# Optimization experiments

Hardware: AMD Instinct MI355X
Metric: run time of the kernel (lower is better)

The kernel has to match this reference:

```python
import jax, jax.numpy as jnp
import numpy as np

B, S, D, H = 2, 2048, 768, 12
HD = D // H  # head dim = 64

def setup_inputs() -> dict:
    key = jax.random.key(0)
    ks = jax.random.split(key, 9)
    s = 1.0 / np.sqrt(D)
    return {
        "x": jax.random.normal(ks[0], (B, S, D), dtype=jnp.float32),
        "Wq": jax.random.uniform(ks[1], (D, D), jnp.float32, -s, s),
        "bq": jax.random.uniform(ks[2], (D,), jnp.float32, -s, s),
        "Wk": jax.random.uniform(ks[3], (D, D), jnp.float32, -s, s),
        "bk": jax.random.uniform(ks[4], (D,), jnp.float32, -s, s),
        "Wv": jax.random.uniform(ks[5], (D, D), jnp.float32, -s, s),
        "bv": jax.random.uniform(ks[6], (D,), jnp.float32, -s, s),
        "Wo": jax.random.uniform(ks[7], (D, D), jnp.float32, -s, s),
        "bo": jax.random.uniform(ks[8], (D,), jnp.float32, -s, s),
    }

def reference(x, Wq, bq, Wk, bk, Wv, bv, Wo, bo):
    b, s, _ = x.shape
    # linear projections, split into heads: [b, h, s, hd]
    def proj(W, bias):
        y = x @ W + bias
        return y.reshape(b, s, H, HD).transpose(0, 2, 1, 3)
    q = proj(Wq, bq)
    k = proj(Wk, bk)
    v = proj(Wv, bv)
    scale = 1.0 / np.sqrt(HD).astype(np.float32)
    scores = jnp.einsum('bhqd,bhkd->bhqk', q, k) * scale
    attn = jax.nn.softmax(scores, axis=-1)
    out = jnp.einsum('bhqk,bhkd->bhqd', attn, v)
    out = out.transpose(0, 2, 1, 3).reshape(b, s, D)
    return out @ Wo + bo
```

## Files before the change

kernel.cpp:

```cpp
#include <hip/hip_runtime.h>
#include <math.h>

#define NH 12
#define SEQ 2048
#define DM 768
#define HD 64
#define NB 2
#define MT (NB * SEQ)
#define QSCL 0.18033688011112042591999058512524f

typedef short bf16x8 __attribute__((ext_vector_type(8)));
typedef float f32x16 __attribute__((ext_vector_type(16)));
typedef unsigned u32x2 __attribute__((ext_vector_type(2)));

__device__ __forceinline__ unsigned short bf16_rne(float x) {
    unsigned u = __float_as_uint(x);
    u += 0x7fffu + ((u >> 16) & 1u);
    return (unsigned short)(u >> 16);
}
__device__ __forceinline__ float bf16_tof(short h) {
    return __uint_as_float(((unsigned)(unsigned short)h) << 16);
}
__device__ __forceinline__ unsigned cvtpk(float lo, float hi) {
    unsigned r;
    asm("v_cvt_pk_bf16_f32 %0, %1, %2" : "=v"(r) : "v"(lo), "v"(hi));
    return r;
}

__device__ __forceinline__ void gl_lds16(const void* g, void* s) {
    __builtin_amdgcn_global_load_lds(
        (const __attribute__((address_space(1))) unsigned int*)g,
        (__attribute__((address_space(3))) unsigned int*)s, 16, 0, 0);
}

__device__ __forceinline__ f32x16 mfma32(bf16x8 a, bf16x8 b, f32x16 c) {
    return __builtin_amdgcn_mfma_f32_32x32x16_bf16(a, b, c, 0, 0, 0);
}

__device__ __forceinline__ bf16x8 gfrag(const char* base, int row, int physblk) {
    return *(const bf16x8*)(base + row * 64 + physblk * 16);
}
__device__ __forceinline__ bf16x8 afrag(const short* base, int row, int blk) {
    return *(const bf16x8*)(base + row * 64 + ((blk ^ (row & 7)) << 3));
}

__global__ __launch_bounds__(256)
void conv_all(const float* __restrict__ x,
              const float* __restrict__ Wq, const float* __restrict__ Wk,
              const float* __restrict__ Wv, const float* __restrict__ Wo,
              short* __restrict__ xg, short* __restrict__ wdst)
{
    int b = blockIdx.x;
    if (b < 1536) {
        const int idx = b * 256 + threadIdx.x;
        const int m = idx / 96, bk = idx % 96;
        const float* src = x + (size_t)m * DM + bk * 8;
        float4 v0 = *(const float4*)src;
        float4 v1 = *(const float4*)(src + 4);
        const float vv[8] = {v0.x, v0.y, v0.z, v0.w, v1.x, v1.y, v1.z, v1.w};
        union { short s[8]; int4 q; } hh;
#pragma unroll
        for (int j = 0; j < 8; j++) hh.s[j] = (short)bf16_rne(vv[j]);
        const int pb = (bk & ~3) | ((bk & 3) ^ ((m >> 1) & 3));
        *(int4*)(xg + (size_t)m * DM + pb * 8) = hh.q;
    } else {
        b -= 1536;
        const int z = b / 288;
        const float* __restrict__ W = (z == 0) ? Wq : (z == 1) ? Wk : (z == 2) ? Wv : Wo;
        const int idx = (b % 288) * 256 + threadIdx.x;
        const int n = idx % 768, bk = idx / 768;
        union { short s[8]; int4 q; } hh;
#pragma unroll
        for (int j = 0; j < 8; j++) hh.s[j] = (short)bf16_rne(W[(size_t)(bk * 8 + j) * DM + n]);
        const int pb = (bk & ~3) | ((bk & 3) ^ ((n >> 1) & 3));
        *(int4*)(wdst + (size_t)z * 589824 + (size_t)n * DM + pb * 8) = hh.q;
    }
}

template<bool SWAP>
__device__ __forceinline__ void qkv_loop(const char* pA, const char* pB,
                                         char* As, char* Bs,
                                         int t, f32x16* acc)
{
    const int w = t >> 6, l = t & 63;
    const int q32 = l & 31, half = l >> 5;
    const int sel = (q32 >> 1) & 3;
    const int arow  = 32 * (w & 1) + q32;
    const int brow0 = 64 * (w >> 1) + q32;
    char* dA = As + t * 16;
    char* dB = Bs + t * 16;

    uint4 a0, b00, b10;
    uint4 a1, b01, b11;

    a0  = *(const uint4*)(pA);
    b00 = *(const uint4*)(pB);
    b10 = *(const uint4*)(pB + 64 * 1536);
    a1  = *(const uint4*)(pA + 64);
    b01 = *(const uint4*)(pB + 64);
    b11 = *(const uint4*)(pB + 64 * 1536 + 64);
    *(uint4*)dA = a0;
    *(uint4*)dB = b00;
    *(uint4*)(dB + 4096) = b10;
    __syncthreads();

    auto compute = [&](const char* sA, const char* sB) {
#pragma unroll
        for (int s = 0; s < 2; s++) {
            const int blk = (s * 2 + half) ^ sel;
            bf16x8 a  = gfrag(sA, arow, blk);
            bf16x8 b0 = gfrag(sB, brow0, blk);
            bf16x8 b1 = gfrag(sB, brow0 + 32, blk);
            if (SWAP) {
                acc[0] = mfma32(b0, a, acc[0]);
                acc[1] = mfma32(b1, a, acc[1]);
            } else {
                acc[0] = mfma32(a, b0, acc[0]);
                acc[1] = mfma32(a, b1, acc[1]);
            }
        }
    };

    for (int kb = 0; kb < 12; kb++) {
        if (kb < 11) {
            const size_t cb = (size_t)(2 * kb + 2) * 64;
            a0  = *(const uint4*)(pA + cb);
            b00 = *(const uint4*)(pB + cb);
            b10 = *(const uint4*)(pB + 64 * 1536 + cb);
        }
        *(uint4*)(dA + 4096) = a1;
        *(uint4*)(dB + 8192) = b01;
        *(uint4*)(dB + 8192 + 4096) = b11;
        compute(As, Bs);
        __syncthreads();

        if (kb < 11) {
            const size_t cb = (size_t)(2 * kb + 3) * 64;
            a1  = *(const uint4*)(pA + cb);
            b01 = *(const uint4*)(pB + cb);
            b11 = *(const uint4*)(pB + 64 * 1536 + cb);
        }
        if (kb < 11) {
            *(uint4*)dA = a0;
            *(uint4*)dB = b00;
            *(uint4*)(dB + 4096) = b10;
        }
        compute(As + 4096, Bs + 8192);
        __syncthreads();
    }
}

__global__ __launch_bounds__(256)
void gemm_qkv(const short* __restrict__ xg, const short* __restrict__ wt,
              const float* __restrict__ bq, const float* __restrict__ bkv,
              const float* __restrict__ bv,
              short* __restrict__ qg, short* __restrict__ kg, short* __restrict__ vg)
{
    const int z = blockIdx.z;
    const short* __restrict__ Bw = wt + (size_t)z * 589824;
    const float* __restrict__ bias = (z == 0) ? bq : (z == 1) ? bkv : bv;

    __shared__ char As[8192], Bs[16384];
    const int t = threadIdx.x, w = t >> 6, l = t & 63;
    const int m0 = blockIdx.y * 64, n0 = blockIdx.x * 128;
    const int q32 = l & 31, half = l >> 5;

    const char* pA = (const char*)xg + (size_t)(m0 + (t >> 2)) * 1536 + (t & 3) * 16;
    const char* pB = (const char*)Bw + (size_t)(n0 + (t >> 2)) * 1536 + (t & 3) * 16;

    f32x16 acc[2];
#pragma unroll
    for (int i = 0; i < 2; i++)
#pragma unroll
        for (int r = 0; r < 16; r++) acc[i][r] = 0.f;

    if (z == 2) {
        qkv_loop<false>(pA, pB, As, Bs, t, acc);
        const int nbase = n0 + 64 * (w >> 1);
        const int h = nbase >> 6;
        const int mbase = m0 + 32 * (w & 1) + 4 * half;
        const int bb = mbase >> 11;
#pragma unroll
        for (int nt = 0; nt < 2; nt++) {
            const int hd = 32 * nt + q32;
            const float bia = bias[nbase + hd];
            short* vrow = vg + ((size_t)(bb * NH + h) * HD + hd) * SEQ;
#pragma unroll
            for (int g = 0; g < 4; g++) {
                const int ss0 = (mbase & 2047) + 8 * g;
                union { unsigned short u[4]; uint2 q; } pk;
#pragma unroll
                for (int j = 0; j < 4; j++)
                    pk.u[j] = bf16_rne(acc[nt][4 * g + j] + bia);
                const int blk = ss0 >> 3;
                const int phys = (blk & ~7) | ((blk & 7) ^ (hd & 7));
                *(uint2*)(vrow + phys * 8 + (ss0 & 7)) = pk.q;
            }
        }
    } else {
        qkv_loop<true>(pA, pB, As, Bs, t, acc);
        short* dst = (z == 0) ? qg : kg;
        const float scl = (z == 0) ? QSCL : 1.0f;
        const int mcol = m0 + 32 * (w & 1) + q32;
        const int bb = mcol >> 11, ss = mcol & 2047;
        const int h = (n0 + 64 * (w >> 1)) >> 6;
        short* drow = dst + ((size_t)(bb * NH + h) * SEQ + ss) * HD;
#pragma unroll
        for (int nt = 0; nt < 2; nt++)
#pragma unroll
            for (int g = 0; g < 4; g++) {
                const int hd0 = 32 * nt + 8 * g + 4 * half;
                float4 b4 = *(const float4*)&bias[(h << 6) + hd0];
                const float bb4[4] = {b4.x, b4.y, b4.z, b4.w};
                union { unsigned short u[4]; uint2 q; } pk;
#pragma unroll
                for (int j = 0; j < 4; j++)
                    pk.u[j] = bf16_rne((acc[nt][4 * g + j] + bb4[j]) * scl);
                const int phys = (hd0 >> 3) ^ (ss & 7);
                *(uint2*)(drow + phys * 8 + (hd0 & 7)) = pk.q;
            }
    }
}

__global__ __launch_bounds__(256)
void attn_mfma(const short* __restrict__ qg, const short* __restrict__ kg,
               const short* __restrict__ vg,
               short* __restrict__ opart, float* __restrict__ lpart)
{
    __shared__ short Qs[8192];
    __shared__ short Ks[4096];
    __shared__ short Vt[4096];

    const int t = threadIdx.x, w = t >> 6, l = t & 63;
    const int bh = blockIdx.y, q0 = blockIdx.x * 128, ks = blockIdx.z;
    const char* qp = (const char*)(qg + (size_t)bh * SEQ * HD);
    const char* kp = (const char*)(kg + (size_t)bh * SEQ * HD);
    const char* vp = (const char*)(vg + (size_t)bh * HD * SEQ);
    const int kbase = ks * 1024;

#pragma unroll
    for (int i = 0; i < 4; i++)
        gl_lds16(qp + (size_t)(q0 + w * 32 + i * 8) * 128 + l * 16,
                 (char*)Qs + (w * 32 + i * 8) * 128);
#pragma unroll
    for (int i = 0; i < 2; i++) {
        gl_lds16(kp + (size_t)(kbase + w * 16 + i * 8) * 128 + l * 16,
                 (char*)Ks + (w * 16 + i * 8) * 128);
        gl_lds16(vp + (size_t)(w * 16 + i * 8 + (l >> 3)) * 4096 + kbase * 2 + (l & 7) * 16,
                 (char*)Vt + (w * 16 + i * 8) * 128);
    }
    __syncthreads();

    const int half = l >> 5;
    const int q = l & 31;
    bf16x8 qf[4];
#pragma unroll
    for (int s = 0; s < 4; s++)
        qf[s] = afrag(Qs, w * 32 + q, half + s * 2);
    __syncthreads();

    f32x16 oacc[2], lacc;
#pragma unroll
    for (int nt = 0; nt < 2; nt++)
#pragma unroll
        for (int r = 0; r < 16; r++) oacc[nt][r] = 0.f;
#pragma unroll
    for (int r = 0; r < 16; r++) lacc[r] = 0.f;

    bf16x8 onesf;
#pragma unroll
    for (int j = 0; j < 8; j++) onesf[j] = (short)0x3F80;

    for (int kti = 0; kti < 16; kti++) {
        const int cur = kti & 1;
        if (kti < 15) {
            const int kb0 = kbase + (kti + 1) * 64;
            char* kd = cur ? (char*)Ks : (char*)Qs;
            char* vd = cur ? (char*)Vt : (char*)(Qs + 4096);
#pragma unroll
            for (int i = 0; i < 2; i++) {
                gl_lds16(kp + (size_t)(kb0 + w * 16 + i * 8) * 128 + l * 16,
                         kd + (w * 16 + i * 8) * 128);
                gl_lds16(vp + (size_t)(w * 16 + i * 8 + (l >> 3)) * 4096 + kb0 * 2 + (l & 7) * 16,
                         vd + (w * 16 + i * 8) * 128);
            }
        }
        const short* kc = cur ? Qs : Ks;
        const short* vc = cur ? Qs + 4096 : Vt;

        f32x16 sacc[2];
#pragma unroll
        for (int nt = 0; nt < 2; nt++)
#pragma unroll
            for (int r = 0; r < 16; r++) sacc[nt][r] = 0.f;
#pragma unroll
        for (int s = 0; s < 4; s++)
#pragma unroll
            for (int nt = 0; nt < 2; nt++) {
                bf16x8 kf = afrag(kc, nt * 32 + q, half + s * 2);
                sacc[nt] = mfma32(kf, qf[s], sacc[nt]);
            }

#pragma unroll
        for (int nt = 0; nt < 2; nt++)
#pragma unroll
            for (int r = 0; r < 16; r++) sacc[nt][r] = exp2f(sacc[nt][r]);

#pragma unroll
        for (int s = 0; s < 4; s++) {
            const int nt = s >> 1;
            const int rb = (s & 1) * 8;
            const unsigned p0 = cvtpk(sacc[nt][rb + 0], sacc[nt][rb + 1]);
            const unsigned p1 = cvtpk(sacc[nt][rb + 2], sacc[nt][rb + 3]);
            const unsigned p2 = cvtpk(sacc[nt][rb + 4], sacc[nt][rb + 5]);
            const unsigned p3 = cvtpk(sacc[nt][rb + 6], sacc[nt][rb + 7]);
            const u32x2 w02 = __builtin_amdgcn_permlane32_swap(p0, p2, false, false);
            const u32x2 w13 = __builtin_amdgcn_permlane32_swap(p1, p3, false, false);
            union { unsigned u[4]; bf16x8 v; } pf;
            pf.u[0] = w02[0];
            pf.u[1] = w13[0];
            pf.u[2] = w02[1];
            pf.u[3] = w13[1];
            lacc = mfma32(pf.v, onesf, lacc);
#pragma unroll
            for (int nt2 = 0; nt2 < 2; nt2++) {
                bf16x8 vf = afrag(vc, nt2 * 32 + q, half + s * 2);
                oacc[nt2] = mfma32(pf.v, vf, oacc[nt2]);
            }
        }
        __syncthreads();
    }

    const size_t base = (size_t)(ks * 24 + bh) * SEQ;
#pragma unroll
    for (int r = 0; r < 16; r++) {
        const int row = q0 + w * 32 + (r & 3) + 8 * (r >> 2) + 4 * half;
#pragma unroll
        for (int nt = 0; nt < 2; nt++)
            opart[(base + row) * 64 + nt * 32 + q] = (short)bf16_rne(oacc[nt][r]);
        if (q == 0) lpart[base + row] = lacc[r];
    }
}

__global__ __launch_bounds__(256)
void attn_reduce(const short* __restrict__ opart, const float* __restrict__ lpart,
                 short* __restrict__ ag)
{
    const int idx = blockIdx.x * 256 + threadIdx.x;
    const int cg = idx & 7, row = idx >> 3;
    const int bh = row >> 11, s = row & 2047;
    union { short s[8]; int4 q; } a, b, o;
    a.q = *(const int4*)(opart + ((size_t)bh * SEQ + s) * 64 + cg * 8);
    b.q = *(const int4*)(opart + ((size_t)(24 + bh) * SEQ + s) * 64 + cg * 8);
    const float inv = 1.0f / (lpart[(size_t)bh * SEQ + s] + lpart[(size_t)(24 + bh) * SEQ + s]);
#pragma unroll
    for (int j = 0; j < 8; j++)
        o.s[j] = (short)bf16_rne((bf16_tof(a.s[j]) + bf16_tof(b.s[j])) * inv);
    const int bb = bh / NH, h = bh % NH;
    const int m = bb * SEQ + s;
    const int blk = h * 8 + cg;
    const int phys = (blk & ~3) | ((blk & 3) ^ ((m >> 1) & 3));
    *(int4*)(ag + (size_t)m * DM + phys * 8) = o.q;
}

__global__ __launch_bounds__(256)
void gemm_out(const short* __restrict__ ag, const short* __restrict__ wt3,
              const float* __restrict__ bias, float* __restrict__ out)
{
    __shared__ char As[8192], Bs[8192];
    const int t = threadIdx.x, w = t >> 6, l = t & 63;
    const int m0 = blockIdx.y * 64, n0 = blockIdx.x * 64;
    const int q32 = l & 31, half = l >> 5;
    const int sel = (q32 >> 1) & 3;

    const char* pA = (const char*)ag  + (size_t)(m0 + (t >> 2)) * 1536 + (t & 3) * 16;
    const char* pB = (const char*)wt3 + (size_t)(n0 + (t >> 2)) * 1536 + (t & 3) * 16;
    char* dA = As + t * 16;
    char* dB = Bs + t * 16;

    const int arow = 32 * (w & 1) + q32;
    const int brow = 32 * (w >> 1) + q32;

    f32x16 acc;
#pragma unroll
    for (int r = 0; r < 16; r++) acc[r] = 0.f;

    uint4 a0, b0, a1, b1;
    a0 = *(const uint4*)(pA);
    b0 = *(const uint4*)(pB);
    a1 = *(const uint4*)(pA + 64);
    b1 = *(const uint4*)(pB + 64);
    *(uint4*)dA = a0;
    *(uint4*)dB = b0;
    __syncthreads();

    for (int kb = 0; kb < 12; kb++) {
        if (kb < 11) {
            const size_t cb = (size_t)(2 * kb + 2) * 64;
            a0 = *(const uint4*)(pA + cb);
            b0 = *(const uint4*)(pB + cb);
        }
        *(uint4*)(dA + 4096) = a1;
        *(uint4*)(dB + 4096) = b1;
#pragma unroll
        for (int s = 0; s < 2; s++) {
            const int blk = (s * 2 + half) ^ sel;
            acc = mfma32(gfrag(Bs, brow, blk), gfrag(As, arow, blk), acc);
        }
        __syncthreads();

        if (kb < 11) {
            const size_t cb = (size_t)(2 * kb + 3) * 64;
            a1 = *(const uint4*)(pA + cb);
            b1 = *(const uint4*)(pB + cb);
        }
        if (kb < 11) {
            *(uint4*)dA = a0;
            *(uint4*)dB = b0;
        }
#pragma unroll
        for (int s = 0; s < 2; s++) {
            const int blk = (s * 2 + half) ^ sel;
            acc = mfma32(gfrag(Bs + 4096, brow, blk), gfrag(As + 4096, arow, blk), acc);
        }
        __syncthreads();
    }

    const int mcol = m0 + 32 * (w & 1) + q32;
    const int nb0 = n0 + 32 * (w >> 1) + 4 * half;
#pragma unroll
    for (int g = 0; g < 4; g++) {
        const int ng = nb0 + 8 * g;
        float4 b4 = *(const float4*)&bias[ng];
        float4 o;
        o.x = acc[4 * g + 0] + b4.x;
        o.y = acc[4 * g + 1] + b4.y;
        o.z = acc[4 * g + 2] + b4.z;
        o.w = acc[4 * g + 3] + b4.w;
        *(float4*)&out[(size_t)mcol * DM + ng] = o;
    }
}

extern "C" void kernel_launch(void* const* d_in, const int* in_sizes, int n_in,
                              void* d_out, int out_size, void* d_ws, size_t ws_size,
                              hipStream_t stream)
{
    const float* x  = (const float*)d_in[0];
    const float* Wq = (const float*)d_in[1];
    const float* bq = (const float*)d_in[2];
    const float* Wk = (const float*)d_in[3];
    const float* bk = (const float*)d_in[4];
    const float* Wv = (const float*)d_in[5];
    const float* bv = (const float*)d_in[6];
    const float* Wo = (const float*)d_in[7];
    const float* bo = (const float*)d_in[8];
    float* out = (float*)d_out;

    const size_t BUF = (size_t)MT * DM;
    short* xg = (short*)d_ws;
    short* qg = xg + BUF;
    short* kg = qg + BUF;
    short* vg = kg + BUF;
    short* ag = vg + BUF;
    short* wt = ag + BUF;
    short* opart = wt + (size_t)4 * 589824;
    float* lpart = (float*)(opart + (size_t)2 * 24 * SEQ * HD);

    conv_all<<<2688, 256, 0, stream>>>(x, Wq, Wk, Wv, Wo, xg, wt);
    gemm_qkv<<<dim3(6, 64, 3), 256, 0, stream>>>(xg, wt, bq, bk, bv, qg, kg, vg);
    attn_mfma<<<dim3(16, 24, 2), 256, 0, stream>>>(qg, kg, vg, opart, lpart);
    attn_reduce<<<1536, 256, 0, stream>>>(opart, lpart, ag);
    gemm_out<<<dim3(12, 64), 256, 0, stream>>>(ag, wt + (size_t)3 * 589824, bo, out);
}
```

Baseline: 192.2 us.

## Triple-buffer K/V tiles in attention with explicit vmcnt waits and MFMA priority

Replaces the double-buffered K/V staging in the attention kernel with a three-slot ring that prefetches two tiles ahead. It uses explicit s_waitcnt vmcnt counts and a single barrier per iteration instead of two __syncthreads. The Q region is reused as a third K/V slot after the Q fragments are read. It also raises wave priority around the MFMA sections with s_setprio to favour matrix issue. The goal is to hide global-to-LDS latency better and cut barrier overhead. The cost is a dependence on hand-counted vmcnt values, which must match the number of outstanding loads exactly.

```diff
diff --git a/kernel.cpp b/kernel.cpp
--- a/kernel.cpp
+++ b/kernel.cpp
@@ -227,9 +227,7 @@
                const short* __restrict__ vg,
                short* __restrict__ opart, float* __restrict__ lpart)
 {
-    __shared__ short Qs[8192];
-    __shared__ short Ks[4096];
-    __shared__ short Vt[4096];
+    __shared__ __align__(16) short lds[24576];
 
     const int t = threadIdx.x, w = t >> 6, l = t & 63;
     const int bh = blockIdx.y, q0 = blockIdx.x * 128, ks = blockIdx.z;
@@ -238,26 +236,36 @@
     const char* vp = (const char*)(vg + (size_t)bh * HD * SEQ);
     const int kbase = ks * 1024;
 
+    short* const slotp0 = lds + 8192;
+    short* const slotp1 = lds + 16384;
+    short* const slotp2 = lds;
+
+    auto stage_kv = [&](int tile, short* dst) {
+        const int kb0 = kbase + tile * 64;
+#pragma unroll
+        for (int i = 0; i < 2; i++) {
+            gl_lds16(kp + (size_t)(kb0 + w * 16 + i * 8) * 128 + l * 16,
+                     (char*)dst + (w * 16 + i * 8) * 128);
+            gl_lds16(vp + (size_t)(w * 16 + i * 8 + (l >> 3)) * 4096 + kb0 * 2 + (l & 7) * 16,
+                     (char*)(dst + 4096) + (w * 16 + i * 8) * 128);
+        }
+    };
+
 #pragma unroll
     for (int i = 0; i < 4; i++)
         gl_lds16(qp + (size_t)(q0 + w * 32 + i * 8) * 128 + l * 16,
-                 (char*)Qs + (w * 32 + i * 8) * 128);
-#pragma unroll
-    for (int i = 0; i < 2; i++) {
-        gl_lds16(kp + (size_t)(kbase + w * 16 + i * 8) * 128 + l * 16,
-                 (char*)Ks + (w * 16 + i * 8) * 128);
-        gl_lds16(vp + (size_t)(w * 16 + i * 8 + (l >> 3)) * 4096 + kbase * 2 + (l & 7) * 16,
-                 (char*)Vt + (w * 16 + i * 8) * 128);
-    }
-    __syncthreads();
+                 (char*)lds + (w * 32 + i * 8) * 128);
+    stage_kv(0, slotp0);
+    stage_kv(1, slotp1);
+
+    asm volatile("s_waitcnt vmcnt(8)" ::: "memory");
 
     const int half = l >> 5;
     const int q = l & 31;
     bf16x8 qf[4];
 #pragma unroll
     for (int s = 0; s < 4; s++)
-        qf[s] = afrag(Qs, w * 32 + q, half + s * 2);
-    __syncthreads();
+        qf[s] = afrag(lds, w * 32 + q, half + s * 2);
 
     f32x16 oacc[2], lacc;
 #pragma unroll
@@ -272,27 +280,25 @@
     for (int j = 0; j < 8; j++) onesf[j] = (short)0x3F80;
 
     for (int kti = 0; kti < 16; kti++) {
-        const int cur = kti & 1;
-        if (kti < 15) {
-            const int kb0 = kbase + (kti + 1) * 64;
-            char* kd = cur ? (char*)Ks : (char*)Qs;
-            char* vd = cur ? (char*)Vt : (char*)(Qs + 4096);
-#pragma unroll
-            for (int i = 0; i < 2; i++) {
-                gl_lds16(kp + (size_t)(kb0 + w * 16 + i * 8) * 128 + l * 16,
-                         kd + (w * 16 + i * 8) * 128);
-                gl_lds16(vp + (size_t)(w * 16 + i * 8 + (l >> 3)) * 4096 + kb0 * 2 + (l & 7) * 16,
-                         vd + (w * 16 + i * 8) * 128);
-            }
-        }
-        const short* kc = cur ? Qs : Ks;
-        const short* vc = cur ? Qs + 4096 : Vt;
+        if (kti < 15) asm volatile("s_waitcnt vmcnt(4) lgkmcnt(0)" ::: "memory");
+        else          asm volatile("s_waitcnt vmcnt(0) lgkmcnt(0)" ::: "memory");
+        __builtin_amdgcn_s_barrier();
+        asm volatile("" ::: "memory");
+
+        if (kti < 14) {
+            short* dst = (kti % 3 == 0) ? slotp2 : (kti % 3 == 1) ? slotp0 : slotp1;
+            stage_kv(kti + 2, dst);
+        }
+        const short* sl = (kti % 3 == 0) ? slotp0 : (kti % 3 == 1) ? slotp1 : slotp2;
+        const short* kc = sl;
+        const short* vc = sl + 4096;
 
         f32x16 sacc[2];
 #pragma unroll
         for (int nt = 0; nt < 2; nt++)
 #pragma unroll
             for (int r = 0; r < 16; r++) sacc[nt][r] = 0.f;
+        __builtin_amdgcn_s_setprio(1);
 #pragma unroll
         for (int s = 0; s < 4; s++)
 #pragma unroll
@@ -300,12 +306,14 @@
                 bf16x8 kf = afrag(kc, nt * 32 + q, half + s * 2);
                 sacc[nt] = mfma32(kf, qf[s], sacc[nt]);
             }
+        __builtin_amdgcn_s_setprio(0);
 
 #pragma unroll
         for (int nt = 0; nt < 2; nt++)
 #pragma unroll
             for (int r = 0; r < 16; r++) sacc[nt][r] = exp2f(sacc[nt][r]);
 
+        __builtin_amdgcn_s_setprio(1);
 #pragma unroll
         for (int s = 0; s < 4; s++) {
             const int nt = s >> 1;
@@ -328,7 +336,7 @@
                 oacc[nt2] = mfma32(pf.v, vf, oacc[nt2]);
             }
         }
-        __syncthreads();
+        __builtin_amdgcn_s_setprio(0);
     }
 
     const size_t base = (size_t)(ks * 24 + bh) * SEQ;
```

Measured after the change: 193.1 us. About the same (+0.5%).

## Split attention keys four ways and reduce partials with fp32 atomics

Applied to the files above, without the earlier changes.

The attention kernel now splits the key range into four chunks instead of two, launching twice as many blocks with half the loop trips each. Partial outputs and softmax denominators are accumulated with fp32 atomicAdd into a global buffer that conv_all zeroes first, replacing the bf16 partial stores and two-way sum. The goal is better occupancy and latency hiding across the GPU. The cost is heavy atomic traffic, a larger fp32 intermediate, extra zeroing work, and reloading Q in every split block.

```diff
diff --git a/kernel.cpp b/kernel.cpp
--- a/kernel.cpp
+++ b/kernel.cpp
@@ -48,8 +48,15 @@
 void conv_all(const float* __restrict__ x,
               const float* __restrict__ Wq, const float* __restrict__ Wk,
               const float* __restrict__ Wv, const float* __restrict__ Wo,
-              short* __restrict__ xg, short* __restrict__ wdst)
-{
+              short* __restrict__ xg, short* __restrict__ wdst,
+              float* __restrict__ zacc)
+{
+    {
+        uint4 z; z.x = z.y = z.z = z.w = 0u;
+        const unsigned ZN = 798720u;
+        for (unsigned i = blockIdx.x * 256u + threadIdx.x; i < ZN; i += 2688u * 256u)
+            ((uint4*)zacc)[i] = z;
+    }
     int b = blockIdx.x;
     if (b < 1536) {
         const int idx = b * 256 + threadIdx.x;
@@ -225,7 +232,7 @@
 __global__ __launch_bounds__(256)
 void attn_mfma(const short* __restrict__ qg, const short* __restrict__ kg,
                const short* __restrict__ vg,
-               short* __restrict__ opart, float* __restrict__ lpart)
+               float* __restrict__ oaccg, float* __restrict__ laccg)
 {
     __shared__ short Qs[8192];
     __shared__ short Ks[4096];
@@ -236,7 +243,7 @@
     const char* qp = (const char*)(qg + (size_t)bh * SEQ * HD);
     const char* kp = (const char*)(kg + (size_t)bh * SEQ * HD);
     const char* vp = (const char*)(vg + (size_t)bh * HD * SEQ);
-    const int kbase = ks * 1024;
+    const int kbase = ks * 512;
 
 #pragma unroll
     for (int i = 0; i < 4; i++)
@@ -271,9 +278,9 @@
 #pragma unroll
     for (int j = 0; j < 8; j++) onesf[j] = (short)0x3F80;
 
-    for (int kti = 0; kti < 16; kti++) {
+    for (int kti = 0; kti < 8; kti++) {
         const int cur = kti & 1;
-        if (kti < 15) {
+        if (kti < 7) {
             const int kb0 = kbase + (kti + 1) * 64;
             char* kd = cur ? (char*)Ks : (char*)Qs;
             char* vd = cur ? (char*)Vt : (char*)(Qs + 4096);
@@ -331,31 +338,32 @@
         __syncthreads();
     }
 
-    const size_t base = (size_t)(ks * 24 + bh) * SEQ;
+    const size_t base = (size_t)bh * SEQ;
 #pragma unroll
     for (int r = 0; r < 16; r++) {
         const int row = q0 + w * 32 + (r & 3) + 8 * (r >> 2) + 4 * half;
 #pragma unroll
         for (int nt = 0; nt < 2; nt++)
-            opart[(base + row) * 64 + nt * 32 + q] = (short)bf16_rne(oacc[nt][r]);
-        if (q == 0) lpart[base + row] = lacc[r];
+            atomicAdd(&oaccg[(base + row) * 64 + nt * 32 + q], oacc[nt][r]);
+        if (q == 0) atomicAdd(&laccg[base + row], lacc[r]);
     }
 }
 
 __global__ __launch_bounds__(256)
-void attn_reduce(const short* __restrict__ opart, const float* __restrict__ lpart,
+void attn_reduce(const float* __restrict__ oaccg, const float* __restrict__ laccg,
                  short* __restrict__ ag)
 {
     const int idx = blockIdx.x * 256 + threadIdx.x;
     const int cg = idx & 7, row = idx >> 3;
     const int bh = row >> 11, s = row & 2047;
-    union { short s[8]; int4 q; } a, b, o;
-    a.q = *(const int4*)(opart + ((size_t)bh * SEQ + s) * 64 + cg * 8);
-    b.q = *(const int4*)(opart + ((size_t)(24 + bh) * SEQ + s) * 64 + cg * 8);
-    const float inv = 1.0f / (lpart[(size_t)bh * SEQ + s] + lpart[(size_t)(24 + bh) * SEQ + s]);
+    float4 o0 = *(const float4*)(oaccg + (size_t)row * 64 + cg * 8);
+    float4 o1 = *(const float4*)(oaccg + (size_t)row * 64 + cg * 8 + 4);
+    const float inv = 1.0f / laccg[row];
+    const float vv[8] = {o0.x, o0.y, o0.z, o0.w, o1.x, o1.y, o1.z, o1.w};
+    union { short s[8]; int4 q; } o;
 #pragma unroll
     for (int j = 0; j < 8; j++)
-        o.s[j] = (short)bf16_rne((bf16_tof(a.s[j]) + bf16_tof(b.s[j])) * inv);
+        o.s[j] = (short)bf16_rne(vv[j] * inv);
     const int bb = bh / NH, h = bh % NH;
     const int m = bb * SEQ + s;
     const int blk = h * 8 + cg;
@@ -463,12 +471,12 @@
     short* vg = kg + BUF;
     short* ag = vg + BUF;
     short* wt = ag + BUF;
-    short* opart = wt + (size_t)4 * 589824;
-    float* lpart = (float*)(opart + (size_t)2 * 24 * SEQ * HD);
-
-    conv_all<<<2688, 256, 0, stream>>>(x, Wq, Wk, Wv, Wo, xg, wt);
+    float* oaccg = (float*)(wt + (size_t)4 * 589824);
+    float* laccg = oaccg + (size_t)24 * SEQ * HD;
+
+    conv_all<<<2688, 256, 0, stream>>>(x, Wq, Wk, Wv, Wo, xg, wt, oaccg);
     gemm_qkv<<<dim3(6, 64, 3), 256, 0, stream>>>(xg, wt, bq, bk, bv, qg, kg, vg);
-    attn_mfma<<<dim3(16, 24, 2), 256, 0, stream>>>(qg, kg, vg, opart, lpart);
-    attn_reduce<<<1536, 256, 0, stream>>>(opart, lpart, ag);
+    attn_mfma<<<dim3(16, 24, 4), 256, 0, stream>>>(qg, kg, vg, oaccg, laccg);
+    attn_reduce<<<1536, 256, 0, stream>>>(oaccg, laccg, ag);
     gemm_out<<<dim3(12, 64), 256, 0, stream>>>(ag, wt + (size_t)3 * 589824, bo, out);
 }
```

After: 227.7 us. 18.5% more time.
